# Kernel tuning notes

Measured on AMD Instinct MI355X. Metric: run time of the kernel, lower is better.

## Reference

```python
import jax, jax.numpy as jnp
import numpy as np

KERNEL_SIZE = 7
NUM_HEADS = 16
CHANNELS = 1024
HEAD_DIM = CHANNELS // NUM_HEADS
PAD = KERNEL_SIZE // 2


def setup_inputs() -> dict:
    key = jax.random.key(0)
    k1, k2 = jax.random.split(key)
    B, S, C = 4, 2048, CHANNELS
    x = jax.random.normal(k1, (B, S, C), dtype=jnp.float32)
    W_pred = jax.random.normal(k2, (C, KERNEL_SIZE * NUM_HEADS), dtype=jnp.float32) * (1.0 / np.sqrt(C))
    b_pred = jnp.zeros((KERNEL_SIZE * NUM_HEADS,), dtype=jnp.float32)
    return {"x": x, "W_pred": W_pred, "b_pred": b_pred}


def reference(x, W_pred, b_pred):
    B, S, C = x.shape
    # per-position kernel prediction: [B,S,H,K]
    kernels = (jnp.einsum('bsc,ck->bsk', x, W_pred) + b_pred).reshape(B, S, NUM_HEADS, KERNEL_SIZE)
    # split channels into heads: [B,S,H,D]
    x_heads = x.reshape(B, S, NUM_HEADS, HEAD_DIM)
    # pad along sequence dim
    x_pad = jnp.pad(x_heads, ((0, 0), (PAD, PAD), (0, 0), (0, 0)))
    # sum over K shifted slices weighted by predicted kernels (K is small, fixed)
    out = jnp.zeros_like(x_heads)
    for i in range(KERNEL_SIZE):
        out = out + kernels[:, :, :, i:i + 1] * jax.lax.dynamic_slice_in_dim(x_pad, i, S, axis=1)
    return out.reshape(B, S, C)
```

## Files before the change

kernel.cpp:

```cpp
#include <hip/hip_runtime.h>
#include <hip/hip_bf16.h>
#include <cstdint>

#define SEQ   2048
#define CH    1024
#define NHEAD 16
#define KSZ   7
#define NCOL  112
#define PADW  3

#define BM       16
#define NTHREADS 256
#define LDK_STR  113
#define NKSTEP   32
#define WS_FRAG_BYTES (NKSTEP * 7 * 64 * 16)

typedef __bf16 v8bf __attribute__((ext_vector_type(8)));
typedef float  v4f  __attribute__((ext_vector_type(4)));

__global__ __launch_bounds__(256)
void prep_w(const float* __restrict__ Wp, __bf16* __restrict__ wsB) {
    const int g  = blockIdx.x * 256 + threadIdx.x;
    const int j  = g & 7;
    const int l  = (g >> 3) & 63;
    const int st = g >> 9;
    const int s  = st / 7;
    const int t  = st - s * 7;
    const int k  = s * 32 + (l >> 4) * 8 + j;
    const int n  = t * 16 + (l & 15);
    wsB[g] = (__bf16)Wp[k * NCOL + n];
}

template <bool PRE>
__global__ __launch_bounds__(NTHREADS, 2)
void dynconv_fused(const float* __restrict__ x,
                   const float* __restrict__ Wp,
                   const float* __restrict__ bp,
                   const __bf16* __restrict__ wsB,
                   float* __restrict__ out)
{
    __shared__ float ldsK[BM * LDK_STR];

    const int tid  = threadIdx.x;
    const int bb   = blockIdx.x;
    const int b    = bb >> 7;
    const int s0   = (bb & 127) << 4;

    const int wave = tid >> 6;
    const int lane = tid & 63;
    const int lq   = lane >> 4;
    const int lm   = lane & 15;

    const float* xbase = x + (size_t)b * SEQ * CH;

    const int tile0 = wave * 2;
    const int tile1 = (wave < 3) ? wave * 2 + 1 : 6;

    v4f acc0 = (v4f){0.f, 0.f, 0.f, 0.f};
    v4f acc1 = (v4f){0.f, 0.f, 0.f, 0.f};

    const float* arow = xbase + (size_t)(s0 + lm) * CH + lq * 8;

    #pragma unroll 8
    for (int s = 0; s < NKSTEP; ++s) {
        const float* p = arow + s * 32;
        const v4f v0 = *(const v4f*)p;
        const v4f v1 = *(const v4f*)(p + 4);
        v8bf af;
        af[0] = (__bf16)v0.x; af[1] = (__bf16)v0.y;
        af[2] = (__bf16)v0.z; af[3] = (__bf16)v0.w;
        af[4] = (__bf16)v1.x; af[5] = (__bf16)v1.y;
        af[6] = (__bf16)v1.z; af[7] = (__bf16)v1.w;

        v8bf bf0, bf1;
        if (PRE) {
            bf0 = *(const v8bf*)&wsB[(size_t)((s * 7 + tile0) * 64 + lane) * 8];
            bf1 = *(const v8bf*)&wsB[(size_t)((s * 7 + tile1) * 64 + lane) * 8];
        } else {
            #pragma unroll
            for (int j = 0; j < 8; ++j) {
                const int k = s * 32 + lq * 8 + j;
                bf0[j] = (__bf16)Wp[k * NCOL + tile0 * 16 + lm];
                bf1[j] = (__bf16)Wp[k * NCOL + tile1 * 16 + lm];
            }
        }
        acc0 = __builtin_amdgcn_mfma_f32_16x16x32_bf16(af, bf0, acc0, 0, 0, 0);
        acc1 = __builtin_amdgcn_mfma_f32_16x16x32_bf16(af, bf1, acc1, 0, 0, 0);
    }

    {
        const int ct0 = tile0 * 16 + lm;
        const float bias0 = bp[ct0];
        #pragma unroll
        for (int r = 0; r < 4; ++r)
            ldsK[(lq * 4 + r) * LDK_STR + ct0] = acc0[r] + bias0;
        if (wave < 3) {
            const int ct1 = tile1 * 16 + lm;
            const float bias1 = bp[ct1];
            #pragma unroll
            for (int r = 0; r < 4; ++r)
                ldsK[(lq * 4 + r) * LDK_STR + ct1] = acc1[r] + bias1;
        }
    }

    const int h  = tid >> 4;
    const int c4 = tid << 2;

    v4f win[BM + 6];
    #pragma unroll
    for (int i = 0; i < BM + 6; ++i) {
        const int sg = s0 - PADW + i;
        win[i] = (sg >= 0 && sg < SEQ)
                     ? *(const v4f*)(xbase + (size_t)sg * CH + c4)
                     : (v4f){0.f, 0.f, 0.f, 0.f};
    }

    __syncthreads();

    float* orow = out + ((size_t)b * SEQ + s0) * CH + c4;
    #pragma unroll
    for (int r = 0; r < BM; ++r) {
        const float* kp = &ldsK[r * LDK_STR + h * KSZ];
        v4f a = (v4f){0.f, 0.f, 0.f, 0.f};
        #pragma unroll
        for (int i = 0; i < KSZ; ++i) {
            a += kp[i] * win[r + i];
        }
        *(v4f*)(orow + (size_t)r * CH) = a;
    }
}

extern "C" void kernel_launch(void* const* d_in, const int* in_sizes, int n_in,
                              void* d_out, int out_size, void* d_ws, size_t ws_size,
                              hipStream_t stream) {
    const float* x  = (const float*)d_in[0];
    const float* Wp = (const float*)d_in[1];
    const float* bp = (const float*)d_in[2];
    float* out = (float*)d_out;

    if (ws_size >= (size_t)WS_FRAG_BYTES) {
        __bf16* wsB = (__bf16*)d_ws;
        prep_w<<<dim3(448), dim3(256), 0, stream>>>(Wp, wsB);
        dynconv_fused<true><<<dim3(512), dim3(NTHREADS), 0, stream>>>(x, Wp, bp, wsB, out);
    } else {
        dynconv_fused<false><<<dim3(512), dim3(NTHREADS), 0, stream>>>(x, Wp, bp, nullptr, out);
    }
}
```

Measured before the change: 104.7 us.

## Stage bf16 weight fragments through LDS in-kernel instead of prep kernel

```diff
diff --git a/kernel.cpp b/kernel.cpp
--- a/kernel.cpp
+++ b/kernel.cpp
@@ -13,33 +13,23 @@
 #define NTHREADS 256
 #define LDK_STR  113
 #define NKSTEP   32
-#define WS_FRAG_BYTES (NKSTEP * 7 * 64 * 16)
+#define KSTAGE   4
+#define NSTAGE   (NKSTEP / KSTAGE)
+#define ROWS_PER_STAGE (KSTAGE * 32)
+#define TASKS_PER_STAGE ((ROWS_PER_STAGE/8) * NCOL)
+#define TASKS_PER_THREAD (TASKS_PER_STAGE / NTHREADS)
 
 typedef __bf16 v8bf __attribute__((ext_vector_type(8)));
 typedef float  v4f  __attribute__((ext_vector_type(4)));
 
-__global__ __launch_bounds__(256)
-void prep_w(const float* __restrict__ Wp, __bf16* __restrict__ wsB) {
-    const int g  = blockIdx.x * 256 + threadIdx.x;
-    const int j  = g & 7;
-    const int l  = (g >> 3) & 63;
-    const int st = g >> 9;
-    const int s  = st / 7;
-    const int t  = st - s * 7;
-    const int k  = s * 32 + (l >> 4) * 8 + j;
-    const int n  = t * 16 + (l & 15);
-    wsB[g] = (__bf16)Wp[k * NCOL + n];
-}
-
-template <bool PRE>
 __global__ __launch_bounds__(NTHREADS, 2)
 void dynconv_fused(const float* __restrict__ x,
                    const float* __restrict__ Wp,
                    const float* __restrict__ bp,
-                   const __bf16* __restrict__ wsB,
                    float* __restrict__ out)
 {
     __shared__ float ldsK[BM * LDK_STR];
+    __shared__ alignas(16) __bf16 wlds[KSTAGE * 7 * 64 * 8];
 
     const int tid  = threadIdx.x;
     const int bb   = blockIdx.x;
@@ -61,31 +51,44 @@
 
     const float* arow = xbase + (size_t)(s0 + lm) * CH + lq * 8;
 
-    #pragma unroll 8
-    for (int s = 0; s < NKSTEP; ++s) {
-        const float* p = arow + s * 32;
-        const v4f v0 = *(const v4f*)p;
-        const v4f v1 = *(const v4f*)(p + 4);
-        v8bf af;
-        af[0] = (__bf16)v0.x; af[1] = (__bf16)v0.y;
-        af[2] = (__bf16)v0.z; af[3] = (__bf16)v0.w;
-        af[4] = (__bf16)v1.x; af[5] = (__bf16)v1.y;
-        af[6] = (__bf16)v1.z; af[7] = (__bf16)v1.w;
+    for (int st = 0; st < NSTAGE; ++st) {
+        if (st) __syncthreads();
 
-        v8bf bf0, bf1;
-        if (PRE) {
-            bf0 = *(const v8bf*)&wsB[(size_t)((s * 7 + tile0) * 64 + lane) * 8];
-            bf1 = *(const v8bf*)&wsB[(size_t)((s * 7 + tile1) * 64 + lane) * 8];
-        } else {
+        #pragma unroll
+        for (int t = 0; t < TASKS_PER_THREAD; ++t) {
+            const int task = t * NTHREADS + tid;
+            const int g8   = task / NCOL;
+            const int n    = task - g8 * NCOL;
+            const int k0   = st * ROWS_PER_STAGE + g8 * 8;
+            const int sloc = g8 >> 2;
+            const int lqw  = g8 & 3;
+            const float* wp = Wp + (size_t)k0 * NCOL + n;
+            v8bf bv;
             #pragma unroll
-            for (int j = 0; j < 8; ++j) {
-                const int k = s * 32 + lq * 8 + j;
-                bf0[j] = (__bf16)Wp[k * NCOL + tile0 * 16 + lm];
-                bf1[j] = (__bf16)Wp[k * NCOL + tile1 * 16 + lm];
-            }
+            for (int j = 0; j < 8; ++j)
+                bv[j] = (__bf16)wp[(size_t)j * NCOL];
+            const int gran = (sloc * 7 + (n >> 4)) * 64 + lqw * 16 + (n & 15);
+            *(v8bf*)&wlds[(size_t)gran * 8] = bv;
         }
-        acc0 = __builtin_amdgcn_mfma_f32_16x16x32_bf16(af, bf0, acc0, 0, 0, 0);
-        acc1 = __builtin_amdgcn_mfma_f32_16x16x32_bf16(af, bf1, acc1, 0, 0, 0);
+        __syncthreads();
+
+        #pragma unroll
+        for (int ss = 0; ss < KSTAGE; ++ss) {
+            const int s = st * KSTAGE + ss;
+            const float* p = arow + s * 32;
+            const v4f v0 = *(const v4f*)p;
+            const v4f v1 = *(const v4f*)(p + 4);
+            v8bf af;
+            af[0] = (__bf16)v0.x; af[1] = (__bf16)v0.y;
+            af[2] = (__bf16)v0.z; af[3] = (__bf16)v0.w;
+            af[4] = (__bf16)v1.x; af[5] = (__bf16)v1.y;
+            af[6] = (__bf16)v1.z; af[7] = (__bf16)v1.w;
+
+            const v8bf bf0 = *(const v8bf*)&wlds[(size_t)((ss*7 + tile0)*64 + lane)*8];
+            const v8bf bf1 = *(const v8bf*)&wlds[(size_t)((ss*7 + tile1)*64 + lane)*8];
+            acc0 = __builtin_amdgcn_mfma_f32_16x16x32_bf16(af, bf0, acc0, 0, 0, 0);
+            acc1 = __builtin_amdgcn_mfma_f32_16x16x32_bf16(af, bf1, acc1, 0, 0, 0);
+        }
     }
 
     {
@@ -137,12 +140,7 @@
     const float* Wp = (const float*)d_in[1];
     const float* bp = (const float*)d_in[2];
     float* out = (float*)d_out;
+    (void)d_ws; (void)ws_size;
 
-    if (ws_size >= (size_t)WS_FRAG_BYTES) {
-        __bf16* wsB = (__bf16*)d_ws;
-        prep_w<<<dim3(448), dim3(256), 0, stream>>>(Wp, wsB);
-        dynconv_fused<true><<<dim3(512), dim3(NTHREADS), 0, stream>>>(x, Wp, bp, wsB, out);
-    } else {
-        dynconv_fused<false><<<dim3(512), dim3(NTHREADS), 0, stream>>>(x, Wp, bp, nullptr, out);
-    }
+    dynconv_fused<<<dim3(512), dim3(NTHREADS), 0, stream>>>(x, Wp, bp, out);
 }
```

After: 107.1 us. 1.02x slower.
